# Optimization experiments

Hardware: AMD Instinct MI355X
Metric: run time of the kernel (lower is better)

## Reference

```python
import jax, jax.numpy as jnp
import numpy as np

B, H, N, D = 2, 16, 4096, 64
NUM_PROJS = 8
BLOCK_SIZE = 256
SAMPLE_SIZE = 256
SCALE = D ** -0.5  # default scale = dim ** -0.5


def _unit_hamming_distance_array(size_n):
    # Gray-code permutation so that adjacent hash buckets differ in one bit
    a = np.array([0, 1], dtype=np.int32)
    for _ in range(size_n - 1):
        a = np.concatenate([a, np.flip(a) + a.shape[0]])
    return a

_PERM = jnp.asarray(_unit_hamming_distance_array(NUM_PROJS))
_ENC = jnp.asarray(2 ** np.arange(NUM_PROJS, dtype=np.int32))  # [num_projs]


def lsh_hash(x, proj_dir):
    # x: [b,h,n,d], proj_dir: [d,r] -> bucket id per token: [b,h,n]
    proj = jnp.einsum('bhnd,dr->bhnr', x, proj_dir)
    bin_ids = jnp.sum((proj > 0).astype(jnp.int32) * _ENC, axis=-1)
    return _PERM[bin_ids]


def attn_lse(q, k, v, scale):
    # exact softmax attention returning output and log-sum-exp
    s = jnp.einsum('...md,...nd->...mn', q, k) * scale
    lse = jax.nn.logsumexp(s, axis=-1, keepdims=True)
    out = jnp.einsum('...mn,...nv->...mv', jnp.exp(s - lse), v)
    return out, lse


def gather_seq(x, idx):
    # gather along the sequence axis (axis=2); broadcasts over last dim
    return jnp.take_along_axis(x, idx[..., None], axis=2)


def add_self_attentions(attn1, lse1, attn2, lse2):
    # combine two un-normalized softmax attentions via their lse's
    c = jax.nn.sigmoid(lse1 - lse2)  # = 1/(1+exp(lse2-lse1))
    attn = c * attn1 + (1.0 - c) * attn2
    lse = jnp.logaddexp(lse1, lse2)
    return attn, lse


def setup_inputs() -> dict:
    key = jax.random.key(0)
    kq, kk, kv, kp, ks = jax.random.split(key, 5)
    return {
        'query': jax.random.normal(kq, (B, H, N, D), jnp.float32),
        'key': jax.random.normal(kk, (B, H, N, D), jnp.float32),
        'value': jax.random.normal(kv, (B, H, N, D), jnp.float32),
        'proj_dir': jax.random.normal(kp, (D, NUM_PROJS), jnp.float32),
        'sampled_set': jax.random.randint(ks, (B, H, SAMPLE_SIZE), 0, N, dtype=jnp.int32),
    }


def reference(query, key, value, proj_dir, sampled_set):
    # --- LSH bucketing + stable sort of queries/keys by bucket id ---
    q_idx = jnp.argsort(lsh_hash(query, proj_dir), axis=2, stable=True)
    k_idx = jnp.argsort(lsh_hash(key, proj_dir), axis=2, stable=True)
    q_idx_inv = jnp.argsort(q_idx, axis=2, stable=True)

    q_s = gather_seq(query, q_idx)
    k_s = gather_seq(key, k_idx)
    v_s = gather_seq(value, k_idx)

    # --- block-diagonal attention in sorted order ---
    nb = N // BLOCK_SIZE
    q_b = q_s.reshape(B, H, nb, BLOCK_SIZE, D)
    k_b = k_s.reshape(B, H, nb, BLOCK_SIZE, D)
    v_b = v_s.reshape(B, H, nb, BLOCK_SIZE, D)
    attn_blk, lse_blk = attn_lse(q_b, k_b, v_b, SCALE)
    attn_blk = attn_blk.reshape(B, H, N, D)
    lse_blk = lse_blk.reshape(B, H, N, 1)
    # un-sort back to original query order
    attn_blk = gather_seq(attn_blk, q_idx_inv)
    lse_blk = gather_seq(lse_blk, q_idx_inv)

    # --- uniformly sampled residual attention, importance-weighted ---
    k_sub = gather_seq(key, sampled_set)
    v_sub = gather_seq(value, sampled_set)
    attn_res, lse_res = attn_lse(query, k_sub, v_sub, SCALE)
    lse_res = lse_res + jnp.log(N / SAMPLE_SIZE)

    attn, lse = add_self_attentions(attn_blk, lse_blk, attn_res, lse_res)
    return attn
```

## Files before the change

### kernel.cpp

```cpp
#include <hip/hip_runtime.h>
#include <hip/hip_bf16.h>
#include <math.h>

#define BH_ 32
#define N_ 4096
#define D_ 64
#define SAMP_ 256
#define SCALE_ 0.125f
#define LOG16_ 2.7725887222397811f
#define HPAD 68

typedef __attribute__((ext_vector_type(4))) float f32x4;
typedef __attribute__((ext_vector_type(8))) short bf16x8;
typedef __attribute__((ext_vector_type(4))) short bf16x4;

static __device__ __forceinline__ unsigned pack2(float a, float b) {
    union { __hip_bfloat162 h; unsigned u; } c;
    c.h = __float22bfloat162_rn(make_float2(a, b));
    return c.u;
}

static __device__ __forceinline__ bf16x8 cvt8v(f32x4 a, f32x4 b) {
    union { unsigned u[4]; bf16x8 v; } r;
    r.u[0] = pack2(a[0], a[1]); r.u[1] = pack2(a[2], a[3]);
    r.u[2] = pack2(b[0], b[1]); r.u[3] = pack2(b[2], b[3]);
    return r.v;
}

static __device__ __forceinline__ bf16x8 cvt8(const float* p) {
    return cvt8v(*(const f32x4*)p, *(const f32x4*)(p + 4));
}

__global__ __launch_bounds__(128) void hash_kernel(
    const float* __restrict__ q, const float* __restrict__ k,
    const float* __restrict__ pd,
    unsigned char* __restrict__ qbuck, unsigned char* __restrict__ kbuck)
{
    extern __shared__ char smraw[];
    float*  Xs  = (float*)smraw;
    double* Pdl = (double*)(smraw + 128 * HPAD * 4);

    int tid = threadIdx.x;
    const float* src = blockIdx.y ? k : q;
    unsigned char* dst = blockIdx.y ? kbuck : qbuck;
    size_t tok0 = (size_t)blockIdx.x * 128;

    {
        int d = tid >> 1, r0 = (tid & 1) * 4;
#pragma unroll
        for (int j = 0; j < 4; ++j)
            Pdl[d * 8 + r0 + j] = (double)pd[d * 8 + r0 + j];
    }
    {
        const float4* src4 = (const float4*)(src + tok0 * D_);
        for (int i = tid; i < 128 * 16; i += 128) {
            int r = i >> 4, c = i & 15;
            *(float4*)&Xs[r * HPAD + c * 4] = src4[i];
        }
    }
    __syncthreads();

    float xr[64];
#pragma unroll
    for (int c = 0; c < 16; ++c)
        *(f32x4*)&xr[c * 4] = *(const f32x4*)&Xs[tid * HPAD + c * 4];

    double acc[8];
#pragma unroll
    for (int r = 0; r < 8; ++r) acc[r] = 0.0;
#pragma unroll
    for (int d = 0; d < 64; ++d) {
        double x = (double)xr[d];
        const double* pr = Pdl + d * 8;
#pragma unroll
        for (int r = 0; r < 8; ++r) acc[r] += x * pr[r];
    }
    int bin = 0;
#pragma unroll
    for (int r = 0; r < 8; ++r)
        if (acc[r] > 0.0) bin |= (1 << r);
    dst[tok0 + tid] = (unsigned char)(bin ^ (bin >> 1));
}

__global__ __launch_bounds__(256) void sort_kernel(
    const unsigned char* __restrict__ qbuck,
    const unsigned char* __restrict__ kbuck,
    int* __restrict__ q_idx, int* __restrict__ k_idx)
{
    __shared__ unsigned short hist[64][256];
    __shared__ unsigned int   binstart[256];
    __shared__ alignas(16) unsigned char bl[N_];

    int bh = blockIdx.x, tensor = blockIdx.y;
    const unsigned char* buck = (tensor ? kbuck : qbuck) + bh * N_;
    int* idx_out = (tensor ? k_idx : q_idx) + bh * N_;
    int t = threadIdx.x;

    ((uint4*)bl)[t] = ((const uint4*)buck)[t];
    {
        uint4* h4 = (uint4*)&hist[0][0];
        for (int i = t; i < 2048; i += 256) h4[i] = make_uint4(0, 0, 0, 0);
    }
    __syncthreads();

    if (t < 64) {
        for (int u = 0; u < 64; ++u) hist[t][bl[t * 64 + u]]++;
    }
    __syncthreads();

    {
        unsigned run = 0;
        for (int tt = 0; tt < 64; ++tt) {
            unsigned c = hist[tt][t];
            hist[tt][t] = (unsigned short)run;
            run += c;
        }
        binstart[t] = run;
    }
    __syncthreads();

    if (t < 64) {
        unsigned b0 = binstart[t*4], b1 = binstart[t*4+1],
                 b2 = binstart[t*4+2], b3 = binstart[t*4+3];
        unsigned s = b0 + b1 + b2 + b3, p = s;
#pragma unroll
        for (int d = 1; d < 64; d <<= 1) {
            unsigned y = __shfl_up(p, d);
            if (t >= d) p += y;
        }
        unsigned e = p - s;
        binstart[t*4]   = e;
        binstart[t*4+1] = e + b0;
        binstart[t*4+2] = e + b0 + b1;
        binstart[t*4+3] = e + b0 + b1 + b2;
    }
    __syncthreads();

    if (t < 64) {
        for (int u = 0; u < 64; ++u) {
            int tok = t * 64 + u;
            int b = bl[tok];
            int pos = (int)(binstart[b] + hist[t][b]);
            hist[t][b]++;
            idx_out[pos] = tok;
        }
    }
}

__global__ __launch_bounds__(512, 4) void fused_attn(
    const float* __restrict__ query, const float* __restrict__ key,
    const float* __restrict__ value, const int* __restrict__ q_idx,
    const int* __restrict__ k_idx, const int* __restrict__ sampled,
    float* __restrict__ out)
{
    __shared__ __align__(16) short Ksm[4096];
    __shared__ __align__(16) short Vsm[4096];
    int wg = blockIdx.x, bh = wg >> 4, blk = wg & 15;
    int tid = threadIdx.x, w = tid >> 6, l = tid & 63, lg = l >> 4, ll = l & 15;
    size_t base = (size_t)bh * N_;

    int krow = tid >> 3, kd8 = tid & 7;
    int kofs = (krow >> 4) * 1024 + (kd8 >> 2) * 512 + (kd8 & 3) * 128 + (krow & 15) * 8;
    int i6 = tid >> 6, l6 = tid & 63;
    int vrow = (i6 >> 2) * 32 + ((l6 >> 5) * 4 + ((l6 >> 1) & 3)) + (i6 & 3) * 8;
    int vd   = (((l6 >> 3) & 3) * 2 + (l6 & 1)) * 8;

    const int* kidxA = k_idx + base + blk * 256;
    const int* kidxB = sampled + bh * SAMP_;

    const int* qidx = q_idx + base + blk * 256 + w * 32;
    int qr[2]; bf16x8 qf[2][2];
#pragma unroll
    for (int mt = 0; mt < 2; ++mt) {
        qr[mt] = qidx[mt * 16 + ll];
        const float* qp = query + (base + (size_t)qr[mt]) * D_;
#pragma unroll
        for (int ks = 0; ks < 2; ++ks)
            qf[mt][ks] = cvt8(qp + ks * 32 + lg * 8);
    }

    f32x4 o[4][2]; float lsum[2];
#pragma unroll
    for (int mt = 0; mt < 2; ++mt) {
        lsum[mt] = 0.f;
#pragma unroll
        for (int dt = 0; dt < 4; ++dt) { f32x4 z = {0.f,0.f,0.f,0.f}; o[dt][mt] = z; }
    }
    unsigned vtr = (unsigned)(unsigned long long)(void*)&Vsm[0] + lg * 512 + ll * 8;

    int kI = kidxA[krow], vI = kidxA[vrow];
    f32x4 pk0, pk1, pv0, pv1;
    {
        const float* kp_ = key + (base + (size_t)kI) * D_ + kd8 * 8;
        pk0 = *(const f32x4*)kp_; pk1 = *(const f32x4*)(kp_ + 4);
        const float* vp_ = value + (base + (size_t)vI) * D_ + vd;
        pv0 = *(const f32x4*)vp_; pv1 = *(const f32x4*)(vp_ + 4);
    }
    int kIn = kidxA[64 + krow], vIn = kidxA[64 + vrow];

    for (int c = 0; c < 8; ++c) {
        *(bf16x8*)&Ksm[kofs]    = cvt8v(pk0, pk1);
        *(bf16x8*)&Vsm[tid * 8] = cvt8v(pv0, pv1);
        __syncthreads();

        if (c < 7) {
            const float* kp_ = key + (base + (size_t)kIn) * D_ + kd8 * 8;
            pk0 = *(const f32x4*)kp_; pk1 = *(const f32x4*)(kp_ + 4);
            const float* vp_ = value + (base + (size_t)vIn) * D_ + vd;
            pv0 = *(const f32x4*)vp_; pv1 = *(const f32x4*)(vp_ + 4);
            if (c < 6) {
                const int* nx = (c + 2 < 4) ? (kidxA + (c + 2) * 64)
                                            : (kidxB + (c - 2) * 64);
                kIn = nx[krow]; vIn = nx[vrow];
            }
        }

        float bias = (c < 4) ? 0.f : LOG16_;
#pragma unroll
        for (int ks2 = 0; ks2 < 2; ++ks2) {
            unsigned pbu[2][4];
            __builtin_amdgcn_s_setprio(1);
#pragma unroll
            for (int t = 0; t < 2; ++t) {
                int kt = ks2 * 2 + t;
                f32x4 s0 = {0.f,0.f,0.f,0.f}, s1 = {0.f,0.f,0.f,0.f};
#pragma unroll
                for (int ks = 0; ks < 2; ++ks) {
                    bf16x8 a = *(const bf16x8*)&Ksm[kt * 1024 + ks * 512 + lg * 128 + ll * 8];
                    s0 = __builtin_amdgcn_mfma_f32_16x16x32_bf16(a, qf[0][ks], s0, 0, 0, 0);
                    s1 = __builtin_amdgcn_mfma_f32_16x16x32_bf16(a, qf[1][ks], s1, 0, 0, 0);
                }
                __builtin_amdgcn_s_setprio(0);
                f32x4 e0, e1;
#pragma unroll
                for (int r = 0; r < 4; ++r) {
                    e0[r] = __expf(fmaf(s0[r], SCALE_, bias));
                    e1[r] = __expf(fmaf(s1[r], SCALE_, bias));
                }
                lsum[0] += (e0[0] + e0[1]) + (e0[2] + e0[3]);
                lsum[1] += (e1[0] + e1[1]) + (e1[2] + e1[3]);
                pbu[0][t*2]   = pack2(e0[0], e0[1]);
                pbu[0][t*2+1] = pack2(e0[2], e0[3]);
                pbu[1][t*2]   = pack2(e1[0], e1[1]);
                pbu[1][t*2+1] = pack2(e1[2], e1[3]);
                __builtin_amdgcn_s_setprio(1);
            }
            bf16x8 pb0, pb1;
            { union { unsigned u[4]; bf16x8 v; } cc;
              cc.u[0]=pbu[0][0]; cc.u[1]=pbu[0][1]; cc.u[2]=pbu[0][2]; cc.u[3]=pbu[0][3]; pb0=cc.v; }
            { union { unsigned u[4]; bf16x8 v; } cc;
              cc.u[0]=pbu[1][0]; cc.u[1]=pbu[1][1]; cc.u[2]=pbu[1][2]; cc.u[3]=pbu[1][3]; pb1=cc.v; }

            bf16x4 tr[4][2];
#pragma unroll
            for (int dt = 0; dt < 4; ++dt) {
                asm volatile("ds_read_b64_tr_b16 %0, %1 offset:%2"
                             : "=v"(tr[dt][0]) : "v"(vtr), "i"(ks2 * 4096 + dt * 128));
                asm volatile("ds_read_b64_tr_b16 %0, %1 offset:%2"
                             : "=v"(tr[dt][1]) : "v"(vtr), "i"(ks2 * 4096 + dt * 128 + 2048));
            }
            asm volatile("s_waitcnt lgkmcnt(0)" ::: "memory");
            __builtin_amdgcn_sched_barrier(0);
#pragma unroll
            for (int dt = 0; dt < 4; ++dt) {
                union { bf16x4 h[2]; bf16x8 v; } va;
                va.h[0] = tr[dt][0]; va.h[1] = tr[dt][1];
                o[dt][0] = __builtin_amdgcn_mfma_f32_16x16x32_bf16(va.v, pb0, o[dt][0], 0, 0, 0);
                o[dt][1] = __builtin_amdgcn_mfma_f32_16x16x32_bf16(va.v, pb1, o[dt][1], 0, 0, 0);
            }
            __builtin_amdgcn_s_setprio(0);
        }

        __builtin_amdgcn_sched_barrier(0);
        __builtin_amdgcn_s_barrier();
        __builtin_amdgcn_sched_barrier(0);
    }

#pragma unroll
    for (int mt = 0; mt < 2; ++mt) {
        float v = lsum[mt];
        v += __shfl_xor(v, 16);
        v += __shfl_xor(v, 32);
        lsum[mt] = v;
    }
#pragma unroll
    for (int mt = 0; mt < 2; ++mt) {
        float dn = 1.f / lsum[mt];
        float* orow = out + (base + (size_t)qr[mt]) * D_ + lg * 4;
#pragma unroll
        for (int dt = 0; dt < 4; ++dt) {
            f32x4 v = o[dt][mt] * dn;
            *(f32x4*)&orow[dt * 16] = v;
        }
    }
}

extern "C" void kernel_launch(void* const* d_in, const int* in_sizes, int n_in,
                              void* d_out, int out_size, void* d_ws, size_t ws_size,
                              hipStream_t stream)
{
    const float* query = (const float*)d_in[0];
    const float* key   = (const float*)d_in[1];
    const float* value = (const float*)d_in[2];
    const float* pd    = (const float*)d_in[3];
    const int*   samp  = (const int*)d_in[4];
    float* out = (float*)d_out;

    char* ws = (char*)d_ws;
    unsigned char* qbuck = (unsigned char*)ws;
    unsigned char* kbuck = qbuck + (size_t)BH_ * N_;
    int* q_idx = (int*)(ws + 262144);
    int* k_idx = (int*)(ws + 262144 + 524288);

    size_t hash_lds = 128 * HPAD * 4 + 512 * 8;
    hipLaunchKernelGGL(hash_kernel, dim3(BH_ * N_ / 128, 2), dim3(128),
                       hash_lds, stream, query, key, pd, qbuck, kbuck);
    hipLaunchKernelGGL(sort_kernel, dim3(BH_, 2), dim3(256), 0, stream,
                       qbuck, kbuck, q_idx, k_idx);
    hipLaunchKernelGGL(fused_attn, dim3(512), dim3(512), 0, stream,
                       query, key, value, q_idx, k_idx, samp, out);
}
```

Before: 82.93 us.

## Stage full 256-key blocks into LDS and remap workgroup order

Replaces the eight 64-key chunk loop, which prefetched the next chunk into registers, with two phases. Each phase loads all 256 keys/values of a block into a 4x larger LDS buffer and then computes over them, so there are far fewer barriers. It also swizzles the workgroup-to-(head, block) mapping across the grid. The cost is that global loads no longer overlap compute within a workgroup, and the larger LDS footprint may reduce occupancy.

Result: faster. 79.10 us (-4.6%).

```diff
diff --git a/kernel.cpp b/kernel.cpp
--- a/kernel.cpp
+++ b/kernel.cpp
@@ -147,26 +147,125 @@
     }
 }
 
+static __device__ __forceinline__ void stage_kv(
+    const float* __restrict__ key, const float* __restrict__ value,
+    size_t base, int krI, int v0, int v1, int v2, int v3,
+    int hK, int kwofs, int vd, int tid, short* Ksm, short* Vsm)
+{
+    {
+        const float* kp = key + (base + (size_t)krI) * D_ + hK * 32;
+        f32x4 k0 = *(const f32x4*)kp,        k1 = *(const f32x4*)(kp + 4);
+        f32x4 k2 = *(const f32x4*)(kp + 8),  k3 = *(const f32x4*)(kp + 12);
+        f32x4 k4 = *(const f32x4*)(kp + 16), k5 = *(const f32x4*)(kp + 20);
+        f32x4 k6 = *(const f32x4*)(kp + 24), k7 = *(const f32x4*)(kp + 28);
+        *(bf16x8*)&Ksm[kwofs]       = cvt8v(k0, k1);
+        *(bf16x8*)&Ksm[kwofs + 128] = cvt8v(k2, k3);
+        *(bf16x8*)&Ksm[kwofs + 256] = cvt8v(k4, k5);
+        *(bf16x8*)&Ksm[kwofs + 384] = cvt8v(k6, k7);
+    }
+    {
+        const float* vp0 = value + (base + (size_t)v0) * D_ + vd;
+        const float* vp1 = value + (base + (size_t)v1) * D_ + vd;
+        const float* vp2 = value + (base + (size_t)v2) * D_ + vd;
+        const float* vp3 = value + (base + (size_t)v3) * D_ + vd;
+        f32x4 a0 = *(const f32x4*)vp0, b0 = *(const f32x4*)(vp0 + 4);
+        f32x4 a1 = *(const f32x4*)vp1, b1 = *(const f32x4*)(vp1 + 4);
+        f32x4 a2 = *(const f32x4*)vp2, b2 = *(const f32x4*)(vp2 + 4);
+        f32x4 a3 = *(const f32x4*)vp3, b3 = *(const f32x4*)(vp3 + 4);
+        *(bf16x8*)&Vsm[tid * 8]         = cvt8v(a0, b0);
+        *(bf16x8*)&Vsm[4096 + tid * 8]  = cvt8v(a1, b1);
+        *(bf16x8*)&Vsm[8192 + tid * 8]  = cvt8v(a2, b2);
+        *(bf16x8*)&Vsm[12288 + tid * 8] = cvt8v(a3, b3);
+    }
+}
+
+static __device__ __forceinline__ void compute_256(
+    const short* __restrict__ Ksm, unsigned vtr, float bias,
+    const bf16x8 (&qf)[2][2], int lg, int ll,
+    f32x4 (&o)[4][2], float (&lsum)[2])
+{
+#pragma unroll
+    for (int hgi = 0; hgi < 8; ++hgi) {
+        unsigned pbu[2][4];
+        __builtin_amdgcn_s_setprio(1);
+#pragma unroll
+        for (int t = 0; t < 2; ++t) {
+            int kt = hgi * 2 + t;
+            f32x4 s0 = {0.f,0.f,0.f,0.f}, s1 = {0.f,0.f,0.f,0.f};
+#pragma unroll
+            for (int ks = 0; ks < 2; ++ks) {
+                bf16x8 a = *(const bf16x8*)&Ksm[kt * 1024 + ks * 512 + lg * 128 + ll * 8];
+                s0 = __builtin_amdgcn_mfma_f32_16x16x32_bf16(a, qf[0][ks], s0, 0, 0, 0);
+                s1 = __builtin_amdgcn_mfma_f32_16x16x32_bf16(a, qf[1][ks], s1, 0, 0, 0);
+            }
+            __builtin_amdgcn_s_setprio(0);
+            f32x4 e0, e1;
+#pragma unroll
+            for (int r = 0; r < 4; ++r) {
+                e0[r] = __expf(fmaf(s0[r], SCALE_, bias));
+                e1[r] = __expf(fmaf(s1[r], SCALE_, bias));
+            }
+            lsum[0] += (e0[0] + e0[1]) + (e0[2] + e0[3]);
+            lsum[1] += (e1[0] + e1[1]) + (e1[2] + e1[3]);
+            pbu[0][t*2]   = pack2(e0[0], e0[1]);
+            pbu[0][t*2+1] = pack2(e0[2], e0[3]);
+            pbu[1][t*2]   = pack2(e1[0], e1[1]);
+            pbu[1][t*2+1] = pack2(e1[2], e1[3]);
+            __builtin_amdgcn_s_setprio(1);
+        }
+        bf16x8 pb0, pb1;
+        { union { unsigned u[4]; bf16x8 v; } cc;
+          cc.u[0]=pbu[0][0]; cc.u[1]=pbu[0][1]; cc.u[2]=pbu[0][2]; cc.u[3]=pbu[0][3]; pb0=cc.v; }
+        { union { unsigned u[4]; bf16x8 v; } cc;
+          cc.u[0]=pbu[1][0]; cc.u[1]=pbu[1][1]; cc.u[2]=pbu[1][2]; cc.u[3]=pbu[1][3]; pb1=cc.v; }
+
+        bf16x4 tr[4][2];
+#pragma unroll
+        for (int dt = 0; dt < 4; ++dt) {
+            asm volatile("ds_read_b64_tr_b16 %0, %1 offset:%2"
+                         : "=v"(tr[dt][0]) : "v"(vtr), "i"(hgi * 4096 + dt * 128));
+            asm volatile("ds_read_b64_tr_b16 %0, %1 offset:%2"
+                         : "=v"(tr[dt][1]) : "v"(vtr), "i"(hgi * 4096 + dt * 128 + 2048));
+        }
+        asm volatile("s_waitcnt lgkmcnt(0)" ::: "memory");
+        __builtin_amdgcn_sched_barrier(0);
+#pragma unroll
+        for (int dt = 0; dt < 4; ++dt) {
+            union { bf16x4 h[2]; bf16x8 v; } va;
+            va.h[0] = tr[dt][0]; va.h[1] = tr[dt][1];
+            o[dt][0] = __builtin_amdgcn_mfma_f32_16x16x32_bf16(va.v, pb0, o[dt][0], 0, 0, 0);
+            o[dt][1] = __builtin_amdgcn_mfma_f32_16x16x32_bf16(va.v, pb1, o[dt][1], 0, 0, 0);
+        }
+        __builtin_amdgcn_s_setprio(0);
+    }
+}
+
 __global__ __launch_bounds__(512, 4) void fused_attn(
     const float* __restrict__ query, const float* __restrict__ key,
     const float* __restrict__ value, const int* __restrict__ q_idx,
     const int* __restrict__ k_idx, const int* __restrict__ sampled,
     float* __restrict__ out)
 {
-    __shared__ __align__(16) short Ksm[4096];
-    __shared__ __align__(16) short Vsm[4096];
-    int wg = blockIdx.x, bh = wg >> 4, blk = wg & 15;
+    __shared__ __align__(16) short Ksm[16384];
+    __shared__ __align__(16) short Vsm[16384];
+    int wgid = blockIdx.x;
+    int wg = (wgid & 7) * 64 + (wgid >> 3);
+    int bh = wg >> 4, blk = wg & 15;
     int tid = threadIdx.x, w = tid >> 6, l = tid & 63, lg = l >> 4, ll = l & 15;
     size_t base = (size_t)bh * N_;
 
-    int krow = tid >> 3, kd8 = tid & 7;
-    int kofs = (krow >> 4) * 1024 + (kd8 >> 2) * 512 + (kd8 & 3) * 128 + (krow & 15) * 8;
-    int i6 = tid >> 6, l6 = tid & 63;
-    int vrow = (i6 >> 2) * 32 + ((l6 >> 5) * 4 + ((l6 >> 1) & 3)) + (i6 & 3) * 8;
-    int vd   = (((l6 >> 3) & 3) * 2 + (l6 & 1)) * 8;
-
     const int* kidxA = k_idx + base + blk * 256;
     const int* kidxB = sampled + bh * SAMP_;
+
+    int rK = tid & 255, hK = tid >> 8;
+    int kwofs = (rK >> 4) * 1024 + hK * 512 + (rK & 15) * 8;
+    int l6 = tid & 63, i6 = tid >> 6;
+    int vrow = (i6 >> 2) * 32 + (l6 >> 5) * 4 + ((l6 >> 1) & 3) + (i6 & 3) * 8;
+    int vd   = (((l6 >> 3) & 3) * 2 + (l6 & 1)) * 8;
+
+    int krA = kidxA[rK];
+    int vA0 = kidxA[vrow],       vA1 = kidxA[64 + vrow];
+    int vA2 = kidxA[128 + vrow], vA3 = kidxA[192 + vrow];
 
     const int* qidx = q_idx + base + blk * 256 + w * 32;
     int qr[2]; bf16x8 qf[2][2];
@@ -188,93 +287,19 @@
     }
     unsigned vtr = (unsigned)(unsigned long long)(void*)&Vsm[0] + lg * 512 + ll * 8;
 
-    int kI = kidxA[krow], vI = kidxA[vrow];
-    f32x4 pk0, pk1, pv0, pv1;
-    {
-        const float* kp_ = key + (base + (size_t)kI) * D_ + kd8 * 8;
-        pk0 = *(const f32x4*)kp_; pk1 = *(const f32x4*)(kp_ + 4);
-        const float* vp_ = value + (base + (size_t)vI) * D_ + vd;
-        pv0 = *(const f32x4*)vp_; pv1 = *(const f32x4*)(vp_ + 4);
-    }
-    int kIn = kidxA[64 + krow], vIn = kidxA[64 + vrow];
-
-    for (int c = 0; c < 8; ++c) {
-        *(bf16x8*)&Ksm[kofs]    = cvt8v(pk0, pk1);
-        *(bf16x8*)&Vsm[tid * 8] = cvt8v(pv0, pv1);
-        __syncthreads();
-
-        if (c < 7) {
-            const float* kp_ = key + (base + (size_t)kIn) * D_ + kd8 * 8;
-            pk0 = *(const f32x4*)kp_; pk1 = *(const f32x4*)(kp_ + 4);
-            const float* vp_ = value + (base + (size_t)vIn) * D_ + vd;
-            pv0 = *(const f32x4*)vp_; pv1 = *(const f32x4*)(vp_ + 4);
-            if (c < 6) {
-                const int* nx = (c + 2 < 4) ? (kidxA + (c + 2) * 64)
-                                            : (kidxB + (c - 2) * 64);
-                kIn = nx[krow]; vIn = nx[vrow];
-            }
-        }
-
-        float bias = (c < 4) ? 0.f : LOG16_;
-#pragma unroll
-        for (int ks2 = 0; ks2 < 2; ++ks2) {
-            unsigned pbu[2][4];
-            __builtin_amdgcn_s_setprio(1);
-#pragma unroll
-            for (int t = 0; t < 2; ++t) {
-                int kt = ks2 * 2 + t;
-                f32x4 s0 = {0.f,0.f,0.f,0.f}, s1 = {0.f,0.f,0.f,0.f};
-#pragma unroll
-                for (int ks = 0; ks < 2; ++ks) {
-                    bf16x8 a = *(const bf16x8*)&Ksm[kt * 1024 + ks * 512 + lg * 128 + ll * 8];
-                    s0 = __builtin_amdgcn_mfma_f32_16x16x32_bf16(a, qf[0][ks], s0, 0, 0, 0);
-                    s1 = __builtin_amdgcn_mfma_f32_16x16x32_bf16(a, qf[1][ks], s1, 0, 0, 0);
-                }
-                __builtin_amdgcn_s_setprio(0);
-                f32x4 e0, e1;
-#pragma unroll
-                for (int r = 0; r < 4; ++r) {
-                    e0[r] = __expf(fmaf(s0[r], SCALE_, bias));
-                    e1[r] = __expf(fmaf(s1[r], SCALE_, bias));
-                }
-                lsum[0] += (e0[0] + e0[1]) + (e0[2] + e0[3]);
-                lsum[1] += (e1[0] + e1[1]) + (e1[2] + e1[3]);
-                pbu[0][t*2]   = pack2(e0[0], e0[1]);
-                pbu[0][t*2+1] = pack2(e0[2], e0[3]);
-                pbu[1][t*2]   = pack2(e1[0], e1[1]);
-                pbu[1][t*2+1] = pack2(e1[2], e1[3]);
-                __builtin_amdgcn_s_setprio(1);
-            }
-            bf16x8 pb0, pb1;
-            { union { unsigned u[4]; bf16x8 v; } cc;
-              cc.u[0]=pbu[0][0]; cc.u[1]=pbu[0][1]; cc.u[2]=pbu[0][2]; cc.u[3]=pbu[0][3]; pb0=cc.v; }
-            { union { unsigned u[4]; bf16x8 v; } cc;
-              cc.u[0]=pbu[1][0]; cc.u[1]=pbu[1][1]; cc.u[2]=pbu[1][2]; cc.u[3]=pbu[1][3]; pb1=cc.v; }
-
-            bf16x4 tr[4][2];
-#pragma unroll
-            for (int dt = 0; dt < 4; ++dt) {
-                asm volatile("ds_read_b64_tr_b16 %0, %1 offset:%2"
-                             : "=v"(tr[dt][0]) : "v"(vtr), "i"(ks2 * 4096 + dt * 128));
-                asm volatile("ds_read_b64_tr_b16 %0, %1 offset:%2"
-                             : "=v"(tr[dt][1]) : "v"(vtr), "i"(ks2 * 4096 + dt * 128 + 2048));
-            }
-            asm volatile("s_waitcnt lgkmcnt(0)" ::: "memory");
-            __builtin_amdgcn_sched_barrier(0);
-#pragma unroll
-            for (int dt = 0; dt < 4; ++dt) {
-                union { bf16x4 h[2]; bf16x8 v; } va;
-                va.h[0] = tr[dt][0]; va.h[1] = tr[dt][1];
-                o[dt][0] = __builtin_amdgcn_mfma_f32_16x16x32_bf16(va.v, pb0, o[dt][0], 0, 0, 0);
-                o[dt][1] = __builtin_amdgcn_mfma_f32_16x16x32_bf16(va.v, pb1, o[dt][1], 0, 0, 0);
-            }
-            __builtin_amdgcn_s_setprio(0);
-        }
-
-        __builtin_amdgcn_sched_barrier(0);
-        __builtin_amdgcn_s_barrier();
-        __builtin_amdgcn_sched_barrier(0);
-    }
+    stage_kv(key, value, base, krA, vA0, vA1, vA2, vA3, hK, kwofs, vd, tid, Ksm, Vsm);
+    __syncthreads();
+
+    int krB = kidxB[rK];
+    int vB0 = kidxB[vrow],       vB1 = kidxB[64 + vrow];
+    int vB2 = kidxB[128 + vrow], vB3 = kidxB[192 + vrow];
+
+    compute_256(Ksm, vtr, 0.f, qf, lg, ll, o, lsum);
+    __syncthreads();
+
+    stage_kv(key, value, base, krB, vB0, vB1, vB2, vB3, hK, kwofs, vd, tid, Ksm, Vsm);
+    __syncthreads();
+    compute_256(Ksm, vtr, LOG16_, qf, lg, ll, o, lsum);
 
 #pragma unroll
     for (int mt = 0; mt < 2; ++mt) {
```
